# Performance work log

Measured on AMD Instinct MI355X. Metric: run time of the kernel, lower is better.

## Reference

```python
import jax, jax.numpy as jnp
import numpy as np

B, LQ, LK, D = 4, 2048, 2048, 512
EPS = 1e-8  # torch cosine_similarity eps


def setup_inputs() -> dict:
    key = jax.random.key(0)
    ks = jax.random.split(key, 8)
    s = 1.0 / np.sqrt(D)
    return {
        "query": jax.random.normal(ks[0], (B, LQ, D), jnp.float32),
        "key": jax.random.normal(ks[1], (B, LK, D), jnp.float32),
        "value": jax.random.normal(ks[2], (B, LK, D), jnp.float32),
        "Wq": jax.random.normal(ks[3], (D, D), jnp.float32) * s,
        "bq": jax.random.normal(ks[4], (D,), jnp.float32) * s,
        "Wk": jax.random.normal(ks[5], (D, D), jnp.float32) * s,
        "bk": jax.random.normal(ks[6], (D,), jnp.float32) * s,
        "scoring_weights": jnp.ones((3,), jnp.float32) / 3.0,
    }


def reference(query, key, value, Wq, bq, Wk, bk, scoring_weights):
    # fused tanh-QK transforms (torch Linear: x @ W.T + b)
    q = jnp.tanh(jnp.einsum('bqd,ed->bqe', query, Wq) + bq)  # [B,LQ,D]
    k = jnp.tanh(jnp.einsum('bkd,ed->bke', key, Wk) + bk)    # [B,LK,D]

    dot = jnp.einsum('bqd,bkd->bqk', q, k)                   # [B,LQ,LK]
    qn = jnp.linalg.norm(q, axis=-1)                         # [B,LQ]
    kn = jnp.linalg.norm(k, axis=-1)                         # [B,LK]
    # cosine_similarity: dot / max(|q|*|k|, eps)
    cos = dot / jnp.maximum(qn[:, :, None] * kn[:, None, :], EPS)
    # -cdist (p=2): sqrt(|q|^2 + |k|^2 - 2 q.k), clamped at 0
    sq = jnp.maximum(qn[:, :, None] ** 2 + kn[:, None, :] ** 2 - 2.0 * dot, 0.0)
    euc = -jnp.sqrt(sq)

    w = jax.nn.softmax(scoring_weights)
    scores = w[0] * dot + w[1] * cos + w[2] * euc
    attn = jax.nn.softmax(scores, axis=-1)                   # [B,LQ,LK]
    context = jnp.einsum('bqk,bkd->bqd', attn, value)        # [B,LQ,D]
    return context, attn
```

## Files before the change

kernel.cpp:

```cpp
#include <hip/hip_runtime.h>
#include <cstdint>
#include <cstddef>

namespace {

constexpr int BATCH = 4;
constexpr int LQ = 2048;
constexpr int LK = 2048;
constexpr int D = 512;
constexpr int MQ = BATCH * LQ;

using f16 = _Float16;
typedef _Float16 f16x8 __attribute__((ext_vector_type(8)));
typedef _Float16 f16x4 __attribute__((ext_vector_type(4)));
typedef float f32x4 __attribute__((ext_vector_type(4)));

__device__ __forceinline__ f16x8 cvt8(const float4 a, const float4 b) {
  f16x8 h;
  h[0] = (f16)a.x; h[1] = (f16)a.y; h[2] = (f16)a.z; h[3] = (f16)a.w;
  h[4] = (f16)b.x; h[5] = (f16)b.y; h[6] = (f16)b.z; h[7] = (f16)b.w;
  return h;
}

typedef __attribute__((address_space(1))) const void gas_void;
typedef __attribute__((address_space(3))) void las_void;
__device__ __forceinline__ void gload_lds16(const void* g, void* l) {
  __builtin_amdgcn_global_load_lds((gas_void*)g, (las_void*)l, 16, 0, 0);
}

__global__ __launch_bounds__(256) void prep_kernel(
    const float* __restrict__ query, const float* __restrict__ keyp,
    const float* __restrict__ value, const float* __restrict__ Wq,
    const float* __restrict__ Wk, const float* __restrict__ bq,
    const float* __restrict__ bk, f16* __restrict__ qh, f16* __restrict__ kh,
    float* __restrict__ qnsqp, float* __restrict__ knsqp,
    f16* __restrict__ vt) {
  __shared__ __align__(16) char smem[21504];
  const int bid0 = blockIdx.x;
  const int t = threadIdx.x;

  if (bid0 >= 512) {
    const int bid = bid0 - 512;
    const int kt = bid & 31;
    const int dt = (bid >> 5) & 7;
    const int b = bid >> 8;
    const int k0 = kt * 64, d0 = dt * 64;
    f16(*T)[72] = reinterpret_cast<f16(*)[72]>(smem);
#pragma unroll
    for (int i = 0; i < 4; ++i) {
      const int u = t + i * 256;
      const int k = u >> 4;
      const int d4 = (u & 15) << 2;
      float4 x = *reinterpret_cast<const float4*>(
          value + (size_t)(b * LK + k0 + k) * D + d0 + d4);
      T[d4 + 0][k] = (f16)x.x;
      T[d4 + 1][k] = (f16)x.y;
      T[d4 + 2][k] = (f16)x.z;
      T[d4 + 3][k] = (f16)x.w;
    }
    __syncthreads();
#pragma unroll
    for (int i = 0; i < 2; ++i) {
      const int u = t + i * 256;
      const int d = u >> 3;
      const int k8 = (u & 7) << 3;
      f16x8 h = *reinterpret_cast<const f16x8*>(&T[d][k8]);
      *reinterpret_cast<f16x8*>(vt + (size_t)(b * D + d0 + d) * LK + k0 + k8) =
          h;
    }
    return;
  }

  const int which = bid0 >> 8;
  const float* __restrict__ X = which ? keyp : query;
  const float* __restrict__ W = which ? Wk : Wq;
  const float* __restrict__ bias = which ? bk : bq;
  f16* __restrict__ out = which ? kh : qh;
  float* __restrict__ nsqp = which ? knsqp : qnsqp;

  const int bid = bid0 & 255;
  const int tm = bid & 63;
  const int tn = bid >> 6;
  const int brow = tm * 128, bcol = tn * 128;
  const int lane = t & 63;
  const int wid = t >> 6;
  const int wr = (wid >> 1) * 64, wc = (wid & 1) * 64;
  const int lr = lane & 15;
  const int lk = (lane >> 4) << 3;
  const int g4 = (lane >> 4) << 2;

  f16(*As)[40] = reinterpret_cast<f16(*)[40]>(smem);
  f16(*Bs)[40] = reinterpret_cast<f16(*)[40]>(smem + 10240);
  float(*s_ss)[2] = reinterpret_cast<float(*)[2]>(smem + 20480);

  f32x4 acc[4][4] = {};

  for (int k0 = 0; k0 < D; k0 += 32) {
#pragma unroll
    for (int i = 0; i < 2; ++i) {
      const int u = t + i * 256;
      const int r = u >> 2;
      const int c8 = (u & 3) << 3;
      const float4* pa =
          reinterpret_cast<const float4*>(X + (size_t)(brow + r) * D + k0 + c8);
      *reinterpret_cast<f16x8*>(&As[r][c8]) = cvt8(pa[0], pa[1]);
      const float4* pb =
          reinterpret_cast<const float4*>(W + (size_t)(bcol + r) * D + k0 + c8);
      *reinterpret_cast<f16x8*>(&Bs[r][c8]) = cvt8(pb[0], pb[1]);
    }
    __syncthreads();
    f16x8 af[4], bf[4];
#pragma unroll
    for (int m = 0; m < 4; ++m)
      af[m] = *reinterpret_cast<const f16x8*>(&As[wr + m * 16 + lr][lk]);
#pragma unroll
    for (int n = 0; n < 4; ++n)
      bf[n] = *reinterpret_cast<const f16x8*>(&Bs[wc + n * 16 + lr][lk]);
#pragma unroll
    for (int m = 0; m < 4; ++m)
#pragma unroll
      for (int n = 0; n < 4; ++n)
        acc[m][n] =
            __builtin_amdgcn_mfma_f32_16x16x32_f16(bf[n], af[m], acc[m][n], 0, 0, 0);
    __syncthreads();
  }

  float4 bv[4];
#pragma unroll
  for (int n = 0; n < 4; ++n)
    bv[n] = *reinterpret_cast<const float4*>(&bias[bcol + wc + n * 16 + g4]);

#pragma unroll
  for (int m = 0; m < 4; ++m) {
    const int row = brow + wr + m * 16 + lr;
    float ss = 0.f;
#pragma unroll
    for (int n = 0; n < 4; ++n) {
      float th[4];
#pragma unroll
      for (int r = 0; r < 4; ++r) {
        th[r] = tanhf(acc[m][n][r] + ((const float*)&bv[n])[r]);
        ss = fmaf(th[r], th[r], ss);
      }
      f16x4 h4;
      h4[0] = (f16)th[0]; h4[1] = (f16)th[1];
      h4[2] = (f16)th[2]; h4[3] = (f16)th[3];
      *reinterpret_cast<f16x4*>(out + (size_t)row * D + bcol + wc + n * 16 + g4) =
          h4;
    }
    ss += __shfl_xor(ss, 16);
    ss += __shfl_xor(ss, 32);
    if (lane < 16) s_ss[wr + m * 16 + lr][wid & 1] = ss;
  }
  __syncthreads();
  if (t < 128) nsqp[(size_t)(brow + t) * 4 + tn] = s_ss[t][0] + s_ss[t][1];
}

template <bool RAW16>
__global__ __launch_bounds__(256, 2) void scores_kernel(
    const f16* __restrict__ qh, const f16* __restrict__ kh,
    const float* __restrict__ qnsqp, const float* __restrict__ knsqp,
    const float* __restrict__ sw, float* __restrict__ attn,
    f16* __restrict__ sraw, float2* __restrict__ tstats) {
  const int bid0 = blockIdx.x;
  const int bid = (bid0 & 7) * 128 + (bid0 >> 3);
  const int tn = bid & 15;
  const int tm = (bid >> 4) & 15;
  const int b = bid >> 8;
  const int brow = tm * 128, bcol = tn * 128;
  const int t = threadIdx.x;
  const int lane = t & 63;
  const int wid = t >> 6;
  const int wr = (wid >> 1) * 64, wc = (wid & 1) * 64;
  const int lr = lane & 15;
  const int lk = (lane >> 4) << 3;
  const int g4 = (lane >> 4) << 2;

  __shared__ f16 As[128 * 64];
  __shared__ f16 Bs[128 * 64];
  __shared__ float s_m[128][2];
  __shared__ float s_l[128][2];

  f32x4 acc[4][4] = {};

  const int srow = lane >> 3;
  const int scol = ((lane & 7) ^ srow) << 4;
  const char* aBase = (const char*)(qh + (size_t)(b * LQ + brow) * D);
  const char* bBase = (const char*)(kh + (size_t)(b * LK + bcol) * D);
  const int swz = (lr & 7) << 4;

  for (int k0 = 0; k0 < D; k0 += 64) {
#pragma unroll
    for (int i = 0; i < 4; ++i) {
      const int chunk = wid * 4 + i;
      const int row = chunk * 8 + srow;
      gload_lds16(aBase + (size_t)row * (D * 2) + k0 * 2 + scol,
                  (char*)As + chunk * 1024);
      gload_lds16(bBase + (size_t)row * (D * 2) + k0 * 2 + scol,
                  (char*)Bs + chunk * 1024);
    }
    __syncthreads();
    f16x8 af[2][4], bf[2][4];
#pragma unroll
    for (int h = 0; h < 2; ++h) {
      const int cb = h * 64 + lk * 2;
#pragma unroll
      for (int m = 0; m < 4; ++m)
        af[h][m] = *(const f16x8*)((const char*)As + (wr + m * 16 + lr) * 128 +
                                   (cb ^ swz));
#pragma unroll
      for (int n = 0; n < 4; ++n)
        bf[h][n] = *(const f16x8*)((const char*)Bs + (wc + n * 16 + lr) * 128 +
                                   (cb ^ swz));
    }
#pragma unroll
    for (int h = 0; h < 2; ++h)
#pragma unroll
      for (int m = 0; m < 4; ++m)
#pragma unroll
        for (int n = 0; n < 4; ++n)
          acc[m][n] = __builtin_amdgcn_mfma_f32_16x16x32_f16(bf[h][n], af[h][m],
                                                             acc[m][n], 0, 0, 0);
    __syncthreads();
  }

  const float s0 = sw[0], s1 = sw[1], s2 = sw[2];
  const float smx = fmaxf(s0, fmaxf(s1, s2));
  float w0 = __expf(s0 - smx), w1 = __expf(s1 - smx), w2 = __expf(s2 - smx);
  const float winv = 1.f / (w0 + w1 + w2);
  w0 *= winv; w1 *= winv; w2 *= winv;

  float qn2_[4], w1rq[4];
#pragma unroll
  for (int m = 0; m < 4; ++m) {
    const float4 qp = *reinterpret_cast<const float4*>(
        &qnsqp[(size_t)(b * LQ + brow + wr + m * 16 + lr) * 4]);
    const float v = (qp.x + qp.y) + (qp.z + qp.w);
    qn2_[m] = v;
    w1rq[m] = w1 * rsqrtf(fmaxf(v, 1e-16f));
  }
  float kn2[4][4], rk[4][4];
#pragma unroll
  for (int n = 0; n < 4; ++n) {
#pragma unroll
    for (int r = 0; r < 4; ++r) {
      const int col = bcol + wc + n * 16 + g4 + r;
      const float4 kp = *reinterpret_cast<const float4*>(
          &knsqp[(size_t)(b * LK + col) * 4]);
      const float v = (kp.x + kp.y) + (kp.z + kp.w);
      kn2[n][r] = v;
      rk[n][r] = rsqrtf(fmaxf(v, 1e-16f));
    }
  }

#pragma unroll
  for (int m = 0; m < 4; ++m) {
    const int row = brow + wr + m * 16 + lr;
    float mx = -3.4e38f;
#pragma unroll
    for (int n = 0; n < 4; ++n) {
      float4 o;
#pragma unroll
      for (int r = 0; r < 4; ++r) {
        const float dot = acc[m][n][r];
        const float qk2 = qn2_[m] + kn2[n][r];
        const float st = sqrtf(fmaxf(qk2 - 2.f * dot, 0.f));
        const float c = fmaf(w1rq[m], rk[n][r], w0);
        const float s = fmaf(dot, c, -w2 * st);
        ((float*)&o)[r] = s;
        acc[m][n][r] = s;
        mx = fmaxf(mx, s);
      }
      if constexpr (RAW16) {
        f16x4 h4;
        h4[0] = (f16)o.x; h4[1] = (f16)o.y; h4[2] = (f16)o.z; h4[3] = (f16)o.w;
        *reinterpret_cast<f16x4*>(sraw + (size_t)(b * LQ + row) * LK + bcol +
                                  wc + n * 16 + g4) = h4;
      } else {
        *reinterpret_cast<float4*>(attn + (size_t)(b * LQ + row) * LK + bcol +
                                   wc + n * 16 + g4) = o;
      }
    }
    mx = fmaxf(mx, __shfl_xor(mx, 16));
    mx = fmaxf(mx, __shfl_xor(mx, 32));
    float es = 0.f;
#pragma unroll
    for (int n = 0; n < 4; ++n)
#pragma unroll
      for (int r = 0; r < 4; ++r) es += __expf(acc[m][n][r] - mx);
    es += __shfl_xor(es, 16);
    es += __shfl_xor(es, 32);
    if (lane < 16) {
      s_m[wr + m * 16 + lr][wid & 1] = mx;
      s_l[wr + m * 16 + lr][wid & 1] = es;
    }
  }
  __syncthreads();
  if (t < 128) {
    const float m0 = s_m[t][0], m1 = s_m[t][1];
    const float M = fmaxf(m0, m1);
    const float L = s_l[t][0] * __expf(m0 - M) + s_l[t][1] * __expf(m1 - M);
    tstats[(size_t)(b * LQ + brow + t) * 16 + tn] = make_float2(M, L);
  }
}

__global__ __launch_bounds__(256) void normalize_kernel(
    float* __restrict__ attn, const float2* __restrict__ tstats) {
  const int row = blockIdx.x;
  const int t = threadIdx.x;
  __shared__ float sM, sI;
  if (t < 16) {
    float2 st = tstats[(size_t)row * 16 + t];
    float M = st.x;
    M = fmaxf(M, __shfl_xor(M, 8));
    M = fmaxf(M, __shfl_xor(M, 4));
    M = fmaxf(M, __shfl_xor(M, 2));
    M = fmaxf(M, __shfl_xor(M, 1));
    float l = st.y * __expf(st.x - M);
    l += __shfl_xor(l, 8);
    l += __shfl_xor(l, 4);
    l += __shfl_xor(l, 2);
    l += __shfl_xor(l, 1);
    if (t == 0) { sM = M; sI = 1.f / l; }
  }
  __syncthreads();
  const float M = sM, invL = sI;
  float* rp = attn + (size_t)row * LK + t * 8;
  float4 v0 = *reinterpret_cast<const float4*>(rp);
  float4 v1 = *reinterpret_cast<const float4*>(rp + 4);
  v0.x = __expf(v0.x - M) * invL; v0.y = __expf(v0.y - M) * invL;
  v0.z = __expf(v0.z - M) * invL; v0.w = __expf(v0.w - M) * invL;
  v1.x = __expf(v1.x - M) * invL; v1.y = __expf(v1.y - M) * invL;
  v1.z = __expf(v1.z - M) * invL; v1.w = __expf(v1.w - M) * invL;
  *reinterpret_cast<float4*>(rp) = v0;
  *reinterpret_cast<float4*>(rp + 4) = v1;
}

template <bool NORM>
__global__ __launch_bounds__(256, 2) void pv_kernel(
    float* __restrict__ attnf, const f16* __restrict__ sraw,
    const f16* __restrict__ vt, const float2* __restrict__ tstats,
    float* __restrict__ ctx) {
  const int bid0 = blockIdx.x;
  const int bid = (bid0 & 7) * 64 + (bid0 >> 3);
  const int tn = bid & 3;
  const int tm = (bid >> 2) & 31;
  const int b = bid >> 7;
  const int brow = tm * 64, bcol = tn * 128;
  const int t = threadIdx.x;
  const int lane = t & 63;
  const int wid = t >> 6;
  const int wr = (wid >> 1) * 32, wc = (wid & 1) * 64;
  const int lr = lane & 15;
  const int lk = (lane >> 4) << 3;
  const int g4 = (lane >> 4) << 2;

  __shared__ f16 As[64 * 64];
  __shared__ f16 Bs[128 * 64];
  __shared__ float sMl[64], sIl[64];

  f32x4 acc[2][4] = {};

  const int srow = lane >> 3;
  const int scol = ((lane & 7) ^ srow) << 4;
  const size_t arow0 = (size_t)(b * LQ + brow);
  const char* bBase = (const char*)(vt + (size_t)(b * D + bcol) * LK);
  const int swz = (lr & 7) << 4;

  float M0 = 0.f, I0 = 0.f, M1 = 0.f, I1 = 0.f;
  if constexpr (NORM) {
    const int prow = t >> 2;
    const int j4 = (t & 3) * 4;
    const float4* tp = reinterpret_cast<const float4*>(
        &tstats[(arow0 + prow) * 16 + j4]);
    const float4 a = tp[0], c = tp[1];
    float m_ = fmaxf(fmaxf(a.x, a.z), fmaxf(c.x, c.z));
    m_ = fmaxf(m_, __shfl_xor(m_, 1));
    m_ = fmaxf(m_, __shfl_xor(m_, 2));
    float l_ = a.y * __expf(a.x - m_) + a.w * __expf(a.z - m_) +
               c.y * __expf(c.x - m_) + c.w * __expf(c.z - m_);
    l_ += __shfl_xor(l_, 1);
    l_ += __shfl_xor(l_, 2);
    if ((t & 3) == 0) {
      sMl[prow] = m_;
      sIl[prow] = 1.f / l_;
    }
    __syncthreads();
    const int r0 = t >> 3;
    M0 = sMl[r0]; I0 = sIl[r0];
    M1 = sMl[r0 + 32]; I1 = sIl[r0 + 32];
  }

  for (int k0 = 0; k0 < LK; k0 += 64) {
    if constexpr (NORM) {
#pragma unroll
      for (int i = 0; i < 2; ++i) {
        const int u = t + i * 256;
        const int row = u >> 3;
        const int c16 = (u & 7) << 4;
        const int csrc = c16 ^ ((row & 7) << 4);
        const float Mr = i ? M1 : M0;
        const float Ir = i ? I1 : I0;
        f16x8 h = *(const f16x8*)((const char*)sraw +
                                  ((arow0 + row) * LK + k0) * 2 + csrc);
        float4 e0, e1;
        e0.x = __expf((float)h[0] - Mr) * Ir;
        e0.y = __expf((float)h[1] - Mr) * Ir;
        e0.z = __expf((float)h[2] - Mr) * Ir;
        e0.w = __expf((float)h[3] - Mr) * Ir;
        e1.x = __expf((float)h[4] - Mr) * Ir;
        e1.y = __expf((float)h[5] - Mr) * Ir;
        e1.z = __expf((float)h[6] - Mr) * Ir;
        e1.w = __expf((float)h[7] - Mr) * Ir;
        *(f16x8*)((char*)As + row * 128 + c16) = cvt8(e0, e1);
        if (tn == 0) {
          float* op = attnf + (arow0 + row) * LK + k0 + (csrc >> 1);
          *reinterpret_cast<float4*>(op) = e0;
          *reinterpret_cast<float4*>(op + 4) = e1;
        }
      }
    } else {
#pragma unroll
      for (int i = 0; i < 2; ++i) {
        const int u = t + i * 256;
        const int row = u >> 3;
        const int c16 = (u & 7) << 4;
        const int csrc = c16 ^ ((row & 7) << 4);
        const float4* ps = (const float4*)((const char*)attnf +
                                           ((arow0 + row) * LK + k0) * 4 + csrc * 2);
        *(f16x8*)((char*)As + row * 128 + c16) = cvt8(ps[0], ps[1]);
      }
    }
#pragma unroll
    for (int i = 0; i < 4; ++i) {
      const int chunk = wid * 4 + i;
      const int row = chunk * 8 + srow;
      gload_lds16(bBase + (size_t)row * (LK * 2) + k0 * 2 + scol,
                  (char*)Bs + chunk * 1024);
    }
    __syncthreads();
    f16x8 af[2][2], bf[2][4];
#pragma unroll
    for (int h = 0; h < 2; ++h) {
      const int cb = h * 64 + lk * 2;
#pragma unroll
      for (int m = 0; m < 2; ++m)
        af[h][m] = *(const f16x8*)((const char*)As + (wr + m * 16 + lr) * 128 +
                                   (cb ^ swz));
#pragma unroll
      for (int n = 0; n < 4; ++n)
        bf[h][n] = *(const f16x8*)((const char*)Bs + (wc + n * 16 + lr) * 128 +
                                   (cb ^ swz));
    }
#pragma unroll
    for (int h = 0; h < 2; ++h)
#pragma unroll
      for (int m = 0; m < 2; ++m)
#pragma unroll
        for (int n = 0; n < 4; ++n)
          acc[m][n] = __builtin_amdgcn_mfma_f32_16x16x32_f16(bf[h][n], af[h][m],
                                                             acc[m][n], 0, 0, 0);
    __syncthreads();
  }

#pragma unroll
  for (int m = 0; m < 2; ++m) {
    const int row = brow + wr + m * 16 + lr;
    float* rowp = ctx + (size_t)(b * LQ + row) * D + bcol + wc;
#pragma unroll
    for (int n = 0; n < 4; ++n) {
      float4 o;
      o.x = acc[m][n][0]; o.y = acc[m][n][1];
      o.z = acc[m][n][2]; o.w = acc[m][n][3];
      *reinterpret_cast<float4*>(rowp + n * 16 + g4) = o;
    }
  }
}

}

extern "C" void kernel_launch(void* const* d_in, const int* in_sizes, int n_in,
                              void* d_out, int out_size, void* d_ws,
                              size_t ws_size, hipStream_t stream) {
  const float* query = (const float*)d_in[0];
  const float* key = (const float*)d_in[1];
  const float* value = (const float*)d_in[2];
  const float* Wq = (const float*)d_in[3];
  const float* bq = (const float*)d_in[4];
  const float* Wk = (const float*)d_in[5];
  const float* bk = (const float*)d_in[6];
  const float* sw = (const float*)d_in[7];

  float* ctx = (float*)d_out;
  float* attn = (float*)d_out + (size_t)BATCH * LQ * D;

  char* ws = (char*)d_ws;
  f16* vt = (f16*)ws;
  f16* qh = (f16*)(ws + (size_t)(8u << 20));
  f16* kh = (f16*)(ws + (size_t)(16u << 20));
  float* qnsqp = (float*)(ws + (size_t)(24u << 20));
  float* knsqp = qnsqp + (size_t)MQ * 4;
  float2* tstats = (float2*)(ws + (size_t)(25u << 20));
  f16* sraw = (f16*)(ws + (size_t)(26u << 20));
  const size_t ws_needed =
      ((size_t)(26u << 20)) + (size_t)BATCH * LQ * LK * sizeof(f16);
  const bool useA16 = ws_size >= ws_needed;

  prep_kernel<<<1536, 256, 0, stream>>>(query, key, value, Wq, Wk, bq, bk, qh,
                                        kh, qnsqp, knsqp, vt);
  if (useA16) {
    scores_kernel<true><<<1024, 256, 0, stream>>>(qh, kh, qnsqp, knsqp, sw,
                                                  attn, sraw, tstats);
    pv_kernel<true><<<512, 256, 0, stream>>>(attn, sraw, vt, tstats, ctx);
  } else {
    scores_kernel<false><<<1024, 256, 0, stream>>>(qh, kh, qnsqp, knsqp, sw,
                                                   attn, sraw, tstats);
    normalize_kernel<<<MQ, 256, 0, stream>>>(attn, tstats);
    pv_kernel<false><<<512, 256, 0, stream>>>(attn, sraw, vt, tstats, ctx);
  }
}
```

Measured before the change: 120.1 us.

## Halve PV row tile, prefetch next score tile, spread attn writes across column blocks

The PV kernel now uses 32-row query tiles instead of 64, which doubles the grid to 1024 blocks and gives each wave one 16-row MFMA slice. The raw fp16 scores for the next k-step are loaded into registers before the current ones are exponentiated, and the global score read is issued after the V tile's async LDS loads. The fp32 attention write is split so each of the four column blocks writes a quarter of the k range instead of block tn==0 writing everything. The aim is more parallelism and balanced stores. In exchange, V tiles are re-read twice as often and each block does less MFMA work per LDS load.

Result: faster. 108.4 us (-9.8%).

```diff
diff --git a/kernel.cpp b/kernel.cpp
--- a/kernel.cpp
+++ b/kernel.cpp
@@ -342,24 +342,24 @@
     const f16* __restrict__ vt, const float2* __restrict__ tstats,
     float* __restrict__ ctx) {
   const int bid0 = blockIdx.x;
-  const int bid = (bid0 & 7) * 64 + (bid0 >> 3);
+  const int bid = (bid0 & 7) * 128 + (bid0 >> 3);
   const int tn = bid & 3;
-  const int tm = (bid >> 2) & 31;
-  const int b = bid >> 7;
-  const int brow = tm * 64, bcol = tn * 128;
+  const int tm = (bid >> 2) & 63;
+  const int b = bid >> 8;
+  const int brow = tm * 32, bcol = tn * 128;
   const int t = threadIdx.x;
   const int lane = t & 63;
   const int wid = t >> 6;
-  const int wr = (wid >> 1) * 32, wc = (wid & 1) * 64;
+  const int wr = (wid >> 1) * 16, wc = (wid & 1) * 64;
   const int lr = lane & 15;
   const int lk = (lane >> 4) << 3;
   const int g4 = (lane >> 4) << 2;
 
-  __shared__ f16 As[64 * 64];
+  __shared__ f16 As[32 * 64];
   __shared__ f16 Bs[128 * 64];
-  __shared__ float sMl[64], sIl[64];
-
-  f32x4 acc[2][4] = {};
+  __shared__ float sMl[32], sIl[32];
+
+  f32x4 acc[4] = {};
 
   const int srow = lane >> 3;
   const int scol = ((lane & 7) ^ srow) << 4;
@@ -367,70 +367,41 @@
   const char* bBase = (const char*)(vt + (size_t)(b * D + bcol) * LK);
   const int swz = (lr & 7) << 4;
 
-  float M0 = 0.f, I0 = 0.f, M1 = 0.f, I1 = 0.f;
+  const int arow = t >> 3;
+  const int c16 = (t & 7) << 4;
+  const int csrc = c16 ^ ((arow & 7) << 4);
+  const char* aRow =
+      (const char*)sraw + (arow0 + arow) * (size_t)LK * 2 + csrc;
+  float Mr = 0.f, Ir = 0.f;
+
   if constexpr (NORM) {
-    const int prow = t >> 2;
-    const int j4 = (t & 3) * 4;
-    const float4* tp = reinterpret_cast<const float4*>(
-        &tstats[(arow0 + prow) * 16 + j4]);
-    const float4 a = tp[0], c = tp[1];
-    float m_ = fmaxf(fmaxf(a.x, a.z), fmaxf(c.x, c.z));
-    m_ = fmaxf(m_, __shfl_xor(m_, 1));
-    m_ = fmaxf(m_, __shfl_xor(m_, 2));
-    float l_ = a.y * __expf(a.x - m_) + a.w * __expf(a.z - m_) +
-               c.y * __expf(c.x - m_) + c.w * __expf(c.z - m_);
-    l_ += __shfl_xor(l_, 1);
-    l_ += __shfl_xor(l_, 2);
-    if ((t & 3) == 0) {
-      sMl[prow] = m_;
-      sIl[prow] = 1.f / l_;
-    }
-    __syncthreads();
-    const int r0 = t >> 3;
-    M0 = sMl[r0]; I0 = sIl[r0];
-    M1 = sMl[r0 + 32]; I1 = sIl[r0 + 32];
-  }
+    if (t < 128) {
+      const int prow = t >> 2;
+      const int j4 = (t & 3) * 4;
+      const float4* tp =
+          reinterpret_cast<const float4*>(&tstats[(arow0 + prow) * 16 + j4]);
+      const float4 a = tp[0], c = tp[1];
+      float m_ = fmaxf(fmaxf(a.x, a.z), fmaxf(c.x, c.z));
+      m_ = fmaxf(m_, __shfl_xor(m_, 1));
+      m_ = fmaxf(m_, __shfl_xor(m_, 2));
+      float l_ = a.y * __expf(a.x - m_) + a.w * __expf(a.z - m_) +
+                 c.y * __expf(c.x - m_) + c.w * __expf(c.z - m_);
+      l_ += __shfl_xor(l_, 1);
+      l_ += __shfl_xor(l_, 2);
+      if ((t & 3) == 0) {
+        sMl[prow] = m_;
+        sIl[prow] = 1.f / l_;
+      }
+    }
+    __syncthreads();
+    Mr = sMl[arow];
+    Ir = sIl[arow];
+  }
+
+  f16x8 hcur;
+  if constexpr (NORM) hcur = *(const f16x8*)(aRow);
 
   for (int k0 = 0; k0 < LK; k0 += 64) {
-    if constexpr (NORM) {
-#pragma unroll
-      for (int i = 0; i < 2; ++i) {
-        const int u = t + i * 256;
-        const int row = u >> 3;
-        const int c16 = (u & 7) << 4;
-        const int csrc = c16 ^ ((row & 7) << 4);
-        const float Mr = i ? M1 : M0;
-        const float Ir = i ? I1 : I0;
-        f16x8 h = *(const f16x8*)((const char*)sraw +
-                                  ((arow0 + row) * LK + k0) * 2 + csrc);
-        float4 e0, e1;
-        e0.x = __expf((float)h[0] - Mr) * Ir;
-        e0.y = __expf((float)h[1] - Mr) * Ir;
-        e0.z = __expf((float)h[2] - Mr) * Ir;
-        e0.w = __expf((float)h[3] - Mr) * Ir;
-        e1.x = __expf((float)h[4] - Mr) * Ir;
-        e1.y = __expf((float)h[5] - Mr) * Ir;
-        e1.z = __expf((float)h[6] - Mr) * Ir;
-        e1.w = __expf((float)h[7] - Mr) * Ir;
-        *(f16x8*)((char*)As + row * 128 + c16) = cvt8(e0, e1);
-        if (tn == 0) {
-          float* op = attnf + (arow0 + row) * LK + k0 + (csrc >> 1);
-          *reinterpret_cast<float4*>(op) = e0;
-          *reinterpret_cast<float4*>(op + 4) = e1;
-        }
-      }
-    } else {
-#pragma unroll
-      for (int i = 0; i < 2; ++i) {
-        const int u = t + i * 256;
-        const int row = u >> 3;
-        const int c16 = (u & 7) << 4;
-        const int csrc = c16 ^ ((row & 7) << 4);
-        const float4* ps = (const float4*)((const char*)attnf +
-                                           ((arow0 + row) * LK + k0) * 4 + csrc * 2);
-        *(f16x8*)((char*)As + row * 128 + c16) = cvt8(ps[0], ps[1]);
-      }
-    }
 #pragma unroll
     for (int i = 0; i < 4; ++i) {
       const int chunk = wid * 4 + i;
@@ -438,15 +409,39 @@
       gload_lds16(bBase + (size_t)row * (LK * 2) + k0 * 2 + scol,
                   (char*)Bs + chunk * 1024);
     }
-    __syncthreads();
-    f16x8 af[2][2], bf[2][4];
+    if constexpr (NORM) {
+      f16x8 hnext;
+      if (k0 + 64 < LK) hnext = *(const f16x8*)(aRow + (k0 + 64) * 2);
+      float4 e0, e1;
+      e0.x = __expf((float)hcur[0] - Mr) * Ir;
+      e0.y = __expf((float)hcur[1] - Mr) * Ir;
+      e0.z = __expf((float)hcur[2] - Mr) * Ir;
+      e0.w = __expf((float)hcur[3] - Mr) * Ir;
+      e1.x = __expf((float)hcur[4] - Mr) * Ir;
+      e1.y = __expf((float)hcur[5] - Mr) * Ir;
+      e1.z = __expf((float)hcur[6] - Mr) * Ir;
+      e1.w = __expf((float)hcur[7] - Mr) * Ir;
+      *(f16x8*)((char*)As + arow * 128 + c16) = cvt8(e0, e1);
+      if ((k0 >> 9) == tn) {
+        float* op = attnf + (arow0 + arow) * LK + k0 + (csrc >> 1);
+        *reinterpret_cast<float4*>(op) = e0;
+        *reinterpret_cast<float4*>(op + 4) = e1;
+      }
+      hcur = hnext;
+    } else {
+      const int u = t;
+      const int row = u >> 3;
+      const float4* ps = (const float4*)((const char*)attnf +
+                                         ((arow0 + row) * LK + k0) * 4 +
+                                         csrc * 2);
+      *(f16x8*)((char*)As + row * 128 + c16) = cvt8(ps[0], ps[1]);
+    }
+    __syncthreads();
+    f16x8 af[2], bf[2][4];
 #pragma unroll
     for (int h = 0; h < 2; ++h) {
       const int cb = h * 64 + lk * 2;
-#pragma unroll
-      for (int m = 0; m < 2; ++m)
-        af[h][m] = *(const f16x8*)((const char*)As + (wr + m * 16 + lr) * 128 +
-                                   (cb ^ swz));
+      af[h] = *(const f16x8*)((const char*)As + (wr + lr) * 128 + (cb ^ swz));
 #pragma unroll
       for (int n = 0; n < 4; ++n)
         bf[h][n] = *(const f16x8*)((const char*)Bs + (wc + n * 16 + lr) * 128 +
@@ -455,25 +450,20 @@
 #pragma unroll
     for (int h = 0; h < 2; ++h)
 #pragma unroll
-      for (int m = 0; m < 2; ++m)
-#pragma unroll
-        for (int n = 0; n < 4; ++n)
-          acc[m][n] = __builtin_amdgcn_mfma_f32_16x16x32_f16(bf[h][n], af[h][m],
-                                                             acc[m][n], 0, 0, 0);
-    __syncthreads();
-  }
-
-#pragma unroll
-  for (int m = 0; m < 2; ++m) {
-    const int row = brow + wr + m * 16 + lr;
-    float* rowp = ctx + (size_t)(b * LQ + row) * D + bcol + wc;
-#pragma unroll
-    for (int n = 0; n < 4; ++n) {
-      float4 o;
-      o.x = acc[m][n][0]; o.y = acc[m][n][1];
-      o.z = acc[m][n][2]; o.w = acc[m][n][3];
-      *reinterpret_cast<float4*>(rowp + n * 16 + g4) = o;
-    }
+      for (int n = 0; n < 4; ++n)
+        acc[n] = __builtin_amdgcn_mfma_f32_16x16x32_f16(bf[h][n], af[h],
+                                                        acc[n], 0, 0, 0);
+    __syncthreads();
+  }
+
+  const int row = brow + wr + lr;
+  float* rowp = ctx + (size_t)(b * LQ + row) * D + bcol + wc;
+#pragma unroll
+  for (int n = 0; n < 4; ++n) {
+    float4 o;
+    o.x = acc[n][0]; o.y = acc[n][1];
+    o.z = acc[n][2]; o.w = acc[n][3];
+    *reinterpret_cast<float4*>(rowp + n * 16 + g4) = o;
   }
 }
 
@@ -511,11 +501,11 @@
   if (useA16) {
     scores_kernel<true><<<1024, 256, 0, stream>>>(qh, kh, qnsqp, knsqp, sw,
                                                   attn, sraw, tstats);
-    pv_kernel<true><<<512, 256, 0, stream>>>(attn, sraw, vt, tstats, ctx);
+    pv_kernel<true><<<1024, 256, 0, stream>>>(attn, sraw, vt, tstats, ctx);
   } else {
     scores_kernel<false><<<1024, 256, 0, stream>>>(qh, kh, qnsqp, knsqp, sw,
                                                    attn, sraw, tstats);
     normalize_kernel<<<MQ, 256, 0, stream>>>(attn, tstats);
-    pv_kernel<false><<<512, 256, 0, stream>>>(attn, sraw, vt, tstats, ctx);
-  }
-}
+    pv_kernel<false><<<1024, 256, 0, stream>>>(attn, sraw, vt, tstats, ctx);
+  }
+}
```
